# Optimization experiments

Measured on AMD Instinct MI355X. Metric: run time of the kernel, lower is better.

## Reference

```python
import jax, jax.numpy as jnp
import numpy as np


def setup_inputs() -> dict:
    key = jax.random.key(0)
    ks = jax.random.split(key, 9)
    B, S, D, E, I = 4, 2048, 1024, 8, 2048
    sd = 1.0 / np.sqrt(D)
    si = 1.0 / np.sqrt(I)
    return {
        "hidden_states": jax.random.normal(ks[0], (B, S, D), dtype=jnp.float32),
        "gate_w": jax.random.normal(ks[1], (D, E), dtype=jnp.float32) * sd,
        "expert_gate_w": jax.random.normal(ks[2], (E, D, I), dtype=jnp.float32) * sd,
        "expert_up_w": jax.random.normal(ks[3], (E, D, I), dtype=jnp.float32) * sd,
        "expert_down_w": jax.random.normal(ks[4], (E, I, D), dtype=jnp.float32) * si,
        "shared_gate_proj_w": jax.random.normal(ks[5], (D, I), dtype=jnp.float32) * sd,
        "shared_up_w": jax.random.normal(ks[6], (D, I), dtype=jnp.float32) * sd,
        "shared_down_w": jax.random.normal(ks[7], (I, D), dtype=jnp.float32) * si,
        "shared_expert_gate_w": jax.random.normal(ks[8], (D, 1), dtype=jnp.float32) * sd,
        "top_k": 2,
    }


def reference(hidden_states, gate_w, expert_gate_w, expert_up_w, expert_down_w,
              shared_gate_proj_w, shared_up_w, shared_down_w, shared_expert_gate_w,
              top_k):
    B, S, D = hidden_states.shape
    E = gate_w.shape[1]
    x = hidden_states.reshape(-1, D)            # [T, D]
    T = x.shape[0]

    # Router: softmax in fp32, top-k, dense per-token per-expert combine weights.
    gate_vals = x @ gate_w                      # [T, E]
    probs = jax.nn.softmax(gate_vals.astype(jnp.float32), axis=-1)
    top_w, top_i = jax.lax.top_k(probs, top_k)  # [T, K]
    dense_w = jnp.zeros((T, E), dtype=jnp.float32)
    dense_w = dense_w.at[jnp.arange(T)[:, None], top_i].set(top_w)
    dense_w = dense_w.astype(x.dtype)           # zero for unselected experts

    # All experts as batched SwiGLU GEMMs (tokens with zero weight contribute 0).
    g = jnp.einsum('td,edi->eti', x, expert_gate_w)
    u = jnp.einsum('td,edi->eti', x, expert_up_w)
    y = jnp.einsum('eti,eid->etd', jax.nn.silu(g) * u, expert_down_w)  # [E, T, D]
    moe_out = jnp.einsum('etd,te->td', y, dense_w)                      # [T, D]

    # Shared expert with sigmoid gate.
    shared = (jax.nn.silu(x @ shared_gate_proj_w) * (x @ shared_up_w)) @ shared_down_w
    shared = jax.nn.sigmoid(x @ shared_expert_gate_w) * shared

    final = (moe_out + shared).reshape(B, S, D)
    return final, gate_vals
```

## Files before the change

kernel.cpp:

```cpp
#include <hip/hip_runtime.h>

typedef __bf16 bf16x8 __attribute__((ext_vector_type(8)));
typedef float f32x4 __attribute__((ext_vector_type(4)));
typedef float f4 __attribute__((ext_vector_type(4)));
typedef unsigned short us8 __attribute__((ext_vector_type(8)));

#define T_TOK 8192
#define DDIM 1024
#define NEXP 8
#define IDIM 2048
#define NCH 1024
#define RROWS 17408
#define ROWS_TOT (T_TOK + RROWS)

__device__ __forceinline__ unsigned short f2bf(float f) {
    unsigned u = __float_as_uint(f);
    u += 0x7fffu + ((u >> 16) & 1u);
    return (unsigned short)(u >> 16);
}

#define GLDS(src, dst) __builtin_amdgcn_global_load_lds( \
    (const __attribute__((address_space(1))) void*)(src), \
    (__attribute__((address_space(3))) void*)(dst), 16, 0, 0)

__global__ __launch_bounds__(256) void router_kernel(
    const float* __restrict__ x, const float* __restrict__ gate_w,
    const float* __restrict__ sgw, float* __restrict__ gate_out,
    float* __restrict__ wdense, float* __restrict__ sgout)
{
    __shared__ float lgw[DDIM * NEXP];
    __shared__ float lsg[DDIM];
    int tid = threadIdx.x;
    for (int i = tid; i < (DDIM * NEXP) / 4; i += 256)
        ((f4*)lgw)[i] = ((const f4*)gate_w)[i];
    for (int i = tid; i < DDIM / 4; i += 256)
        ((f4*)lsg)[i] = ((const f4*)sgw)[i];
    __syncthreads();

    int wid = tid >> 6, l = tid & 63;
    int t = blockIdx.x * 4 + wid;

    float acc[NEXP];
#pragma unroll
    for (int e = 0; e < NEXP; e++) acc[e] = 0.f;
    float accs = 0.f;
    const float* xr = x + (size_t)t * DDIM;
#pragma unroll
    for (int j = 0; j < 4; j++) {
        int d0 = j * 256 + l * 4;
        f4 xv = *(const f4*)(xr + d0);
#pragma unroll
        for (int c = 0; c < 4; c++) {
            float xd = xv[c];
            int d = d0 + c;
#pragma unroll
            for (int e = 0; e < NEXP; e++) acc[e] += xd * lgw[d * NEXP + e];
            accs += xd * lsg[d];
        }
    }
#pragma unroll
    for (int off = 32; off > 0; off >>= 1) {
#pragma unroll
        for (int e = 0; e < NEXP; e++) acc[e] += __shfl_xor(acc[e], off);
        accs += __shfl_xor(accs, off);
    }
    if (l == 0) {
        float m = acc[0];
        for (int e = 1; e < NEXP; e++) m = fmaxf(m, acc[e]);
        float p[NEXP], s = 0.f;
        for (int e = 0; e < NEXP; e++) { p[e] = __expf(acc[e] - m); s += p[e]; }
        float inv = 1.f / s;
        int i1 = 0; float b1 = p[0];
        for (int e = 1; e < NEXP; e++) if (p[e] > b1) { b1 = p[e]; i1 = e; }
        int i2 = -1; float b2 = -1.f;
        for (int e = 0; e < NEXP; e++) if (e != i1 && p[e] > b2) { b2 = p[e]; i2 = e; }
        for (int e = 0; e < NEXP; e++) {
            gate_out[(size_t)t * NEXP + e] = acc[e];
            float w = (e == i1) ? b1 * inv : (e == i2) ? b2 * inv : 0.f;
            wdense[(size_t)t * NEXP + e] = w;
        }
        sgout[t] = 1.f / (1.f + __expf(-accs));
    }
}

__global__ __launch_bounds__(256) void bucket_kernel(
    const float* __restrict__ wdense, int* __restrict__ list,
    float* __restrict__ wl, int* __restrict__ cnt,
    int* __restrict__ te, int* __restrict__ tp)
{
    int e = blockIdx.x;
    int tid = threadIdx.x, wid = tid >> 6, l = tid & 63;
    __shared__ int wsum[4];
    int base = 0;
    int* le = list + (size_t)e * T_TOK;
    float* we = wl + (size_t)e * T_TOK;
    for (int t0 = 0; t0 < T_TOK; t0 += 256) {
        int tok = t0 + tid;
        float w = wdense[(size_t)tok * NEXP + e];
        bool f = w > 0.f;
        unsigned long long m = __ballot(f);
        int lp = __popcll(m & ((1ull << l) - 1ull));
        if (l == 0) wsum[wid] = __popcll(m);
        __syncthreads();
        int woff = 0;
#pragma unroll
        for (int i = 0; i < 4; i++) if (i < wid) woff += wsum[i];
        int btot = wsum[0] + wsum[1] + wsum[2] + wsum[3];
        if (f) {
            int pos = base + woff + lp;
            le[pos] = tok; we[pos] = w;
            int slot = 0;
            for (int e2 = 0; e2 < e; e2++)
                slot += (wdense[(size_t)tok * NEXP + e2] > 0.f) ? 1 : 0;
            te[tok * 2 + slot] = e;
            tp[tok * 2 + slot] = pos;
        }
        base += btot;
        __syncthreads();
    }
    if (tid == 0) cnt[e] = base;
    int align = (base + 255) & ~255;
    for (int i = base + tid; i < align; i += 256) { le[i] = 0; we[i] = 0.f; }
}

__global__ void scan_kernel(const int* __restrict__ cnt, int* __restrict__ offs)
{
    if (threadIdx.x == 0) {
        int o = 0;
        for (int e = 0; e < NEXP; e++) { offs[e] = o; o += (cnt[e] + 127) & ~127; }
    }
}

__global__ __launch_bounds__(256) void cvt_kernel(
    const float* __restrict__ in, unsigned short* __restrict__ out, int n8)
{
    int i = blockIdx.x * 256 + threadIdx.x;
    if (i >= n8) return;
    const f4* p = (const f4*)in + (size_t)i * 2;
    f4 a = p[0], b = p[1];
    us8 o;
#pragma unroll
    for (int k = 0; k < 4; k++) { o[k] = f2bf(a[k]); o[4 + k] = f2bf(b[k]); }
    *((us8*)out + i) = o;
}

__global__ __launch_bounds__(256) void wcvt_gu_kernel(
    const float* __restrict__ egw, const float* __restrict__ euw,
    const float* __restrict__ sgp, const float* __restrict__ sup,
    unsigned short* __restrict__ pool, int c0)
{
    int j = blockIdx.y;
    int e = j >> 1, s = j & 1;
    const float* src = (e < 8) ? ((s ? euw : egw) + (size_t)e * DDIM * IDIM)
                               : (s ? sup : sgp);
    unsigned short* dst = pool + (size_t)j * NCH * DDIM;
    int tpc = NCH / 64;
    int tci = blockIdx.x % tpc, tri = blockIdx.x / tpc;
    int r0 = tri * 64;
    int cl0 = tci * 64;
    int cg0 = c0 + cl0;

    __shared__ unsigned short lds[64][72];
    int t = threadIdx.x;
    int tr = t >> 4, tcc = (t & 15) * 4;
#pragma unroll
    for (int jj = 0; jj < 4; jj++) {
        int r = tr + jj * 16;
        f4 v = *(const f4*)(src + (size_t)(r0 + r) * IDIM + cg0 + tcc);
#pragma unroll
        for (int k = 0; k < 4; k++) lds[r][tcc + k] = f2bf(v[k]);
    }
    __syncthreads();
    int orow = t >> 2, ss = t & 3;
    us8 v0, v1;
#pragma unroll
    for (int i = 0; i < 8; i++) {
        v0[i] = lds[ss * 16 + i][orow];
        v1[i] = lds[ss * 16 + 8 + i][orow];
    }
    unsigned short* op = dst + (size_t)(cl0 + orow) * DDIM + r0 + ss * 16;
    *(us8*)op = v0; *(us8*)(op + 8) = v1;
}

__global__ __launch_bounds__(256) void wcvt_d_kernel(
    const float* __restrict__ edw, const float* __restrict__ sdw,
    unsigned short* __restrict__ pool)
{
    int j = blockIdx.y;
    const float* src = (j < 8) ? edw + (size_t)j * IDIM * DDIM : sdw;
    unsigned short* dst = pool + (size_t)j * DDIM * IDIM;
    int tpc = DDIM / 64;
    int tci = blockIdx.x % tpc, tri = blockIdx.x / tpc;
    int rg0 = tri * 64;
    int cg0 = tci * 64;

    __shared__ unsigned short lds[64][72];
    int t = threadIdx.x;
    int tr = t >> 4, tcc = (t & 15) * 4;
#pragma unroll
    for (int jj = 0; jj < 4; jj++) {
        int r = tr + jj * 16;
        f4 v = *(const f4*)(src + (size_t)(rg0 + r) * DDIM + cg0 + tcc);
#pragma unroll
        for (int k = 0; k < 4; k++) lds[r][tcc + k] = f2bf(v[k]);
    }
    __syncthreads();
    int orow = t >> 2, ss = t & 3;
    us8 v0, v1;
#pragma unroll
    for (int i = 0; i < 8; i++) {
        v0[i] = lds[ss * 16 + i][orow];
        v1[i] = lds[ss * 16 + 8 + i][orow];
    }
    unsigned short* op = dst + (size_t)(cg0 + orow) * IDIM + rg0 + ss * 16;
    *(us8*)op = v0; *(us8*)(op + 8) = v1;
}

__global__ __launch_bounds__(512, 2) void gemm_gateup8(
    const unsigned short* __restrict__ A, const unsigned short* __restrict__ pool,
    unsigned short* __restrict__ H, const int* __restrict__ listb,
    const int* __restrict__ cnt, const int* __restrict__ offs, int c0)
{
    int z = blockIdx.z;
    const unsigned short *Bg, *Bu; const int* lst; int count, rowb;
    if (z == 0) {
        Bg = pool + (size_t)16 * NCH * DDIM; Bu = pool + (size_t)17 * NCH * DDIM;
        lst = nullptr; count = T_TOK; rowb = 0;
    } else {
        int e = z - 1;
        Bg = pool + (size_t)(e * 2) * NCH * DDIM; Bu = pool + (size_t)(e * 2 + 1) * NCH * DDIM;
        lst = listb + (size_t)e * T_TOK; count = cnt[e]; rowb = T_TOK + offs[e];
    }
    int m0 = blockIdx.y * 256, n0 = blockIdx.x * 128;
    if (m0 >= count) return;
    int climit = (count + 127) & ~127;
    const int NT = DDIM / 64;

    __shared__ unsigned short lds[2][32768];

    int tid = threadIdx.x, wid = tid >> 6, l = tid & 63;
    int wm = wid >> 1, wn = wid & 1;
    int lr = l & 15, lkg = l >> 4;

    int sb = tid & 7, sr = tid >> 3;
    int sk = (sb ^ (sr & 7)) << 3;
    const unsigned short* pa[2][2];
#pragma unroll
    for (int h = 0; h < 2; h++)
#pragma unroll
        for (int j = 0; j < 2; j++) {
            int rr = m0 + h * 128 + j * 64 + sr;
            int ga = lst ? lst[rr] : rr;
            pa[h][j] = A + (size_t)ga * DDIM + sk;
        }
    const unsigned short* pbg = Bg + (size_t)(n0 + sr) * DDIM + sk;
    const unsigned short* pbu = Bu + (size_t)(n0 + sr) * DDIM + sk;

#define GU_ST_A(sbuf, h, t) { \
    GLDS(pa[h][0] + (t) * 64, (sbuf) + (h) * 8192 + tid * 8); \
    GLDS(pa[h][1] + (t) * 64, (sbuf) + (h) * 8192 + 4096 + tid * 8); }
#define GU_ST_BG(sbuf, t) { \
    GLDS(pbg + (t) * 64, (sbuf) + 16384 + tid * 8); \
    GLDS(pbg + (size_t)64 * DDIM + (t) * 64, (sbuf) + 16384 + 4096 + tid * 8); }
#define GU_ST_BU(sbuf, t) { \
    GLDS(pbu + (t) * 64, (sbuf) + 24576 + tid * 8); \
    GLDS(pbu + (size_t)64 * DDIM + (t) * 64, (sbuf) + 24576 + 4096 + tid * 8); }

    {
        unsigned short* s0 = &lds[0][0];
        GU_ST_A(s0, 0, 0); GU_ST_A(s0, 1, 0); GU_ST_BG(s0, 0); GU_ST_BU(s0, 0);
        unsigned short* s1 = &lds[1][0];
        GU_ST_A(s1, 0, 1); GU_ST_A(s1, 1, 1); GU_ST_BG(s1, 1); GU_ST_BU(s1, 1);
    }

    int xorc = (lr & 7) << 3;
    int kx0 = (lkg * 8) ^ xorc;
    int kx1 = (32 + lkg * 8) ^ xorc;
    int aoff[4], boff[4];
#pragma unroll
    for (int mf = 0; mf < 4; mf++) {
        int r = wm * 64 + mf * 16 + lr;
        aoff[mf] = (r >> 7) * 8192 + (r & 127) * 64;
    }
#pragma unroll
    for (int nf = 0; nf < 4; nf++)
        boff[nf] = 16384 + (wn * 64 + nf * 16 + lr) * 64;

    f32x4 zero = {0.f, 0.f, 0.f, 0.f};
    f32x4 accg[4][4], accu[4][4];
#pragma unroll
    for (int m = 0; m < 4; m++)
#pragma unroll
        for (int n = 0; n < 4; n++) { accg[m][n] = zero; accu[m][n] = zero; }

    bf16x8 a[2][2], bg[4][2], bu[4][2];

#pragma unroll 1
    for (int t = 0; t < NT; t++) {
        const unsigned short* cb = &lds[t & 1][0];
        unsigned short* sbuf = &lds[t & 1][0];
        bool stg = (t + 2 < NT);

        if (t == NT - 1) { asm volatile("s_waitcnt vmcnt(0)" ::: "memory"); }
        else             { asm volatile("s_waitcnt vmcnt(8)" ::: "memory"); }
        __builtin_amdgcn_s_barrier();
#pragma unroll
        for (int mf = 0; mf < 2; mf++) {
            a[mf][0] = *(const bf16x8*)(cb + aoff[mf] + kx0);
            a[mf][1] = *(const bf16x8*)(cb + aoff[mf] + kx1);
        }
#pragma unroll
        for (int nf = 0; nf < 2; nf++) {
            bg[nf][0] = *(const bf16x8*)(cb + boff[nf] + kx0);
            bg[nf][1] = *(const bf16x8*)(cb + boff[nf] + kx1);
            bu[nf][0] = *(const bf16x8*)(cb + boff[nf] + 8192 + kx0);
            bu[nf][1] = *(const bf16x8*)(cb + boff[nf] + 8192 + kx1);
        }
        __builtin_amdgcn_s_setprio(1);
#pragma unroll
        for (int kh = 0; kh < 2; kh++)
#pragma unroll
            for (int mf = 0; mf < 2; mf++)
#pragma unroll
                for (int nf = 0; nf < 2; nf++) {
                    accg[mf][nf] = __builtin_amdgcn_mfma_f32_16x16x32_bf16(a[mf][kh], bg[nf][kh], accg[mf][nf], 0, 0, 0);
                    accu[mf][nf] = __builtin_amdgcn_mfma_f32_16x16x32_bf16(a[mf][kh], bu[nf][kh], accu[mf][nf], 0, 0, 0);
                }
        __builtin_amdgcn_s_setprio(0);

        __builtin_amdgcn_s_barrier();
#pragma unroll
        for (int nf = 2; nf < 4; nf++) {
            bg[nf][0] = *(const bf16x8*)(cb + boff[nf] + kx0);
            bg[nf][1] = *(const bf16x8*)(cb + boff[nf] + kx1);
            bu[nf][0] = *(const bf16x8*)(cb + boff[nf] + 8192 + kx0);
            bu[nf][1] = *(const bf16x8*)(cb + boff[nf] + 8192 + kx1);
        }
        __builtin_amdgcn_s_setprio(1);
#pragma unroll
        for (int kh = 0; kh < 2; kh++)
#pragma unroll
            for (int mf = 0; mf < 2; mf++)
#pragma unroll
                for (int nf = 2; nf < 4; nf++) {
                    accg[mf][nf] = __builtin_amdgcn_mfma_f32_16x16x32_bf16(a[mf][kh], bg[nf][kh], accg[mf][nf], 0, 0, 0);
                    accu[mf][nf] = __builtin_amdgcn_mfma_f32_16x16x32_bf16(a[mf][kh], bu[nf][kh], accu[mf][nf], 0, 0, 0);
                }
        __builtin_amdgcn_s_setprio(0);

        __builtin_amdgcn_s_barrier();
#pragma unroll
        for (int mf = 0; mf < 2; mf++) {
            a[mf][0] = *(const bf16x8*)(cb + aoff[2 + mf] + kx0);
            a[mf][1] = *(const bf16x8*)(cb + aoff[2 + mf] + kx1);
        }
        if (stg) { GU_ST_BG(sbuf, t + 2); }
        __builtin_amdgcn_s_setprio(1);
#pragma unroll
        for (int kh = 0; kh < 2; kh++)
#pragma unroll
            for (int mf = 0; mf < 2; mf++)
#pragma unroll
                for (int nf = 0; nf < 2; nf++) {
                    accg[2 + mf][nf] = __builtin_amdgcn_mfma_f32_16x16x32_bf16(a[mf][kh], bg[nf][kh], accg[2 + mf][nf], 0, 0, 0);
                    accu[2 + mf][nf] = __builtin_amdgcn_mfma_f32_16x16x32_bf16(a[mf][kh], bu[nf][kh], accu[2 + mf][nf], 0, 0, 0);
                }
        __builtin_amdgcn_s_setprio(0);

        __builtin_amdgcn_s_barrier();
        if (stg) { GU_ST_BU(sbuf, t + 2); GU_ST_A(sbuf, 0, t + 2); GU_ST_A(sbuf, 1, t + 2); }
        __builtin_amdgcn_s_setprio(1);
#pragma unroll
        for (int kh = 0; kh < 2; kh++)
#pragma unroll
            for (int mf = 0; mf < 2; mf++)
#pragma unroll
                for (int nf = 2; nf < 4; nf++) {
                    accg[2 + mf][nf] = __builtin_amdgcn_mfma_f32_16x16x32_bf16(a[mf][kh], bg[nf][kh], accg[2 + mf][nf], 0, 0, 0);
                    accu[2 + mf][nf] = __builtin_amdgcn_mfma_f32_16x16x32_bf16(a[mf][kh], bu[nf][kh], accu[2 + mf][nf], 0, 0, 0);
                }
        __builtin_amdgcn_s_setprio(0);
    }

#pragma unroll
    for (int mf = 0; mf < 4; mf++) {
        int rbase = m0 + wm * 64 + mf * 16 + lkg * 4;
#pragma unroll
        for (int nf = 0; nf < 4; nf++) {
            int col = c0 + n0 + wn * 64 + nf * 16 + lr;
#pragma unroll
            for (int r = 0; r < 4; r++) {
                int rloc = rbase + r;
                if (rloc < climit) {
                    float g = accg[mf][nf][r], u = accu[mf][nf][r];
                    float hv = g * (1.f / (1.f + __expf(-g))) * u;
                    H[(size_t)(rowb + rloc) * IDIM + col] = f2bf(hv);
                }
            }
        }
    }
}

__global__ __launch_bounds__(512, 2) void gemm_down8(
    const unsigned short* __restrict__ H, const unsigned short* __restrict__ pool,
    unsigned short* __restrict__ Y,
    const float* __restrict__ wlb, const float* __restrict__ sgo,
    const int* __restrict__ cnt, const int* __restrict__ offs)
{
    int z = blockIdx.z;
    const unsigned short* B; const float* coef; int count, rowb;
    if (z == 0) {
        B = pool + (size_t)8 * DDIM * IDIM;
        coef = sgo; count = T_TOK; rowb = 0;
    } else {
        int e = z - 1;
        B = pool + (size_t)e * DDIM * IDIM;
        coef = wlb + (size_t)e * T_TOK;
        count = cnt[e]; rowb = T_TOK + offs[e];
    }
    int m0 = blockIdx.y * 256, n0 = blockIdx.x * 256;
    if (m0 >= count) return;
    int climit = (count + 127) & ~127;
    const int NT = IDIM / 64;

    __shared__ unsigned short lds[2][32768];

    int tid = threadIdx.x, wid = tid >> 6, l = tid & 63;
    int wm = wid >> 2, wn = wid & 3;
    int lr = l & 15, lkg = l >> 4;

    int sb = tid & 7, sr = tid >> 3;
    int sk = (sb ^ (sr & 7)) << 3;
    const unsigned short* pah = H + (size_t)(rowb + m0 + sr) * IDIM + sk;
    const unsigned short* pb  = B + (size_t)(n0 + sr) * IDIM + sk;

#define DN_ST_A(sbuf, h, t) { \
    GLDS(pah + (size_t)((h) * 128) * IDIM + (t) * 64, (sbuf) + (h) * 8192 + tid * 8); \
    GLDS(pah + (size_t)((h) * 128 + 64) * IDIM + (t) * 64, (sbuf) + (h) * 8192 + 4096 + tid * 8); }
#define DN_ST_B(sbuf, h, t) { \
    GLDS(pb + (size_t)((h) * 128) * IDIM + (t) * 64, (sbuf) + 16384 + (h) * 8192 + tid * 8); \
    GLDS(pb + (size_t)((h) * 128 + 64) * IDIM + (t) * 64, (sbuf) + 16384 + (h) * 8192 + 4096 + tid * 8); }

    {
        unsigned short* s0 = &lds[0][0];
        DN_ST_A(s0, 0, 0); DN_ST_A(s0, 1, 0); DN_ST_B(s0, 0, 0); DN_ST_B(s0, 1, 0);
        unsigned short* s1 = &lds[1][0];
        DN_ST_A(s1, 0, 1); DN_ST_A(s1, 1, 1); DN_ST_B(s1, 0, 1); DN_ST_B(s1, 1, 1);
    }

    int xorc = (lr & 7) << 3;
    int kx0 = (lkg * 8) ^ xorc;
    int kx1 = (32 + lkg * 8) ^ xorc;
    int aoff[8], boff[4];
#pragma unroll
    for (int mf = 0; mf < 8; mf++)
        aoff[mf] = wm * 8192 + (mf * 16 + lr) * 64;
#pragma unroll
    for (int nf = 0; nf < 4; nf++)
        boff[nf] = 16384 + (wn * 64 + nf * 16 + lr) * 64;

    f32x4 zero = {0.f, 0.f, 0.f, 0.f};
    f32x4 acc[8][4];
#pragma unroll
    for (int m = 0; m < 8; m++)
#pragma unroll
        for (int n = 0; n < 4; n++) acc[m][n] = zero;

    bf16x8 a[4][2], b[4][2];

#pragma unroll 1
    for (int t = 0; t < NT; t++) {
        const unsigned short* cb = &lds[t & 1][0];
        unsigned short* sbuf = &lds[t & 1][0];
        bool stg = (t + 2 < NT);

        if (t == NT - 1) { asm volatile("s_waitcnt vmcnt(0)" ::: "memory"); }
        else             { asm volatile("s_waitcnt vmcnt(8)" ::: "memory"); }
        __builtin_amdgcn_s_barrier();
#pragma unroll
        for (int mf = 0; mf < 4; mf++) {
            a[mf][0] = *(const bf16x8*)(cb + aoff[mf] + kx0);
            a[mf][1] = *(const bf16x8*)(cb + aoff[mf] + kx1);
        }
#pragma unroll
        for (int nf = 0; nf < 2; nf++) {
            b[nf][0] = *(const bf16x8*)(cb + boff[nf] + kx0);
            b[nf][1] = *(const bf16x8*)(cb + boff[nf] + kx1);
        }
        __builtin_amdgcn_s_setprio(1);
#pragma unroll
        for (int kh = 0; kh < 2; kh++)
#pragma unroll
            for (int mf = 0; mf < 4; mf++)
#pragma unroll
                for (int nf = 0; nf < 2; nf++)
                    acc[mf][nf] = __builtin_amdgcn_mfma_f32_16x16x32_bf16(a[mf][kh], b[nf][kh], acc[mf][nf], 0, 0, 0);
        __builtin_amdgcn_s_setprio(0);

        __builtin_amdgcn_s_barrier();
#pragma unroll
        for (int nf = 2; nf < 4; nf++) {
            b[nf][0] = *(const bf16x8*)(cb + boff[nf] + kx0);
            b[nf][1] = *(const bf16x8*)(cb + boff[nf] + kx1);
        }
        __builtin_amdgcn_s_setprio(1);
#pragma unroll
        for (int kh = 0; kh < 2; kh++)
#pragma unroll
            for (int mf = 0; mf < 4; mf++)
#pragma unroll
                for (int nf = 2; nf < 4; nf++)
                    acc[mf][nf] = __builtin_amdgcn_mfma_f32_16x16x32_bf16(a[mf][kh], b[nf][kh], acc[mf][nf], 0, 0, 0);
        __builtin_amdgcn_s_setprio(0);

        __builtin_amdgcn_s_barrier();
#pragma unroll
        for (int mf = 0; mf < 4; mf++) {
            a[mf][0] = *(const bf16x8*)(cb + aoff[4 + mf] + kx0);
            a[mf][1] = *(const bf16x8*)(cb + aoff[4 + mf] + kx1);
        }
        if (stg) { DN_ST_B(sbuf, 0, t + 2); }
        __builtin_amdgcn_s_setprio(1);
#pragma unroll
        for (int kh = 0; kh < 2; kh++)
#pragma unroll
            for (int mf = 0; mf < 4; mf++)
#pragma unroll
                for (int nf = 0; nf < 2; nf++)
                    acc[4 + mf][nf] = __builtin_amdgcn_mfma_f32_16x16x32_bf16(a[mf][kh], b[nf][kh], acc[4 + mf][nf], 0, 0, 0);
        __builtin_amdgcn_s_setprio(0);

        __builtin_amdgcn_s_barrier();
        if (stg) { DN_ST_B(sbuf, 1, t + 2); DN_ST_A(sbuf, 0, t + 2); DN_ST_A(sbuf, 1, t + 2); }
        __builtin_amdgcn_s_setprio(1);
#pragma unroll
        for (int kh = 0; kh < 2; kh++)
#pragma unroll
            for (int mf = 0; mf < 4; mf++)
#pragma unroll
                for (int nf = 2; nf < 4; nf++)
                    acc[4 + mf][nf] = __builtin_amdgcn_mfma_f32_16x16x32_bf16(a[mf][kh], b[nf][kh], acc[4 + mf][nf], 0, 0, 0);
        __builtin_amdgcn_s_setprio(0);
    }

#pragma unroll
    for (int mf = 0; mf < 8; mf++) {
        int rbase = m0 + wm * 128 + mf * 16 + lkg * 4;
        float cf[4];
#pragma unroll
        for (int r = 0; r < 4; r++) {
            int rloc = rbase + r;
            cf[r] = (rloc < climit) ? coef[rloc] : 0.f;
        }
#pragma unroll
        for (int nf = 0; nf < 4; nf++) {
            int col = n0 + wn * 64 + nf * 16 + lr;
#pragma unroll
            for (int r = 0; r < 4; r++) {
                int rloc = rbase + r;
                if (rloc < climit)
                    Y[(size_t)(rowb + rloc) * DDIM + col] = f2bf(cf[r] * acc[mf][nf][r]);
            }
        }
    }
}

__global__ __launch_bounds__(256) void combine_kernel(
    const unsigned short* __restrict__ Y, const int* __restrict__ te,
    const int* __restrict__ tp, const int* __restrict__ offs,
    float* __restrict__ out)
{
    int t = blockIdx.x * 2 + (threadIdx.x >> 7);
    int c = (threadIdx.x & 127) * 8;
    int e0 = te[2 * t], e1 = te[2 * t + 1];
    size_t r0 = (size_t)T_TOK + offs[e0] + tp[2 * t];
    size_t r1 = (size_t)T_TOK + offs[e1] + tp[2 * t + 1];

    us8 vs = *(const us8*)(Y + (size_t)t * DDIM + c);
    us8 v0 = *(const us8*)(Y + r0 * DDIM + c);
    us8 v1 = *(const us8*)(Y + r1 * DDIM + c);
    f4 o0, o1;
#pragma unroll
    for (int k = 0; k < 4; k++) {
        o0[k] = __uint_as_float((unsigned)vs[k] << 16)
              + __uint_as_float((unsigned)v0[k] << 16)
              + __uint_as_float((unsigned)v1[k] << 16);
        o1[k] = __uint_as_float((unsigned)vs[4 + k] << 16)
              + __uint_as_float((unsigned)v0[4 + k] << 16)
              + __uint_as_float((unsigned)v1[4 + k] << 16);
    }
    float* op = out + (size_t)t * DDIM + c;
    *(f4*)op = o0;
    *(f4*)(op + 4) = o1;
}

extern "C" void kernel_launch(void* const* d_in, const int* in_sizes, int n_in,
                              void* d_out, int out_size, void* d_ws, size_t ws_size,
                              hipStream_t stream)
{
    const float* x   = (const float*)d_in[0];
    const float* gw  = (const float*)d_in[1];
    const float* egw = (const float*)d_in[2];
    const float* euw = (const float*)d_in[3];
    const float* edw = (const float*)d_in[4];
    const float* sgp = (const float*)d_in[5];
    const float* sup = (const float*)d_in[6];
    const float* sdw = (const float*)d_in[7];
    const float* seg = (const float*)d_in[8];

    float* out0 = (float*)d_out;
    float* gate_out = out0 + (size_t)T_TOK * DDIM;

    char* ws = (char*)d_ws;
    auto take = [&](size_t bytes) { char* p = ws; ws += (bytes + 255) & ~(size_t)255; return p; };
    unsigned short* xb   = (unsigned short*)take((size_t)T_TOK * DDIM * 2);
    float* wdense = (float*)take((size_t)T_TOK * NEXP * 4);
    float* sgo    = (float*)take((size_t)T_TOK * 4);
    int*   list   = (int*)take((size_t)NEXP * T_TOK * 4);
    float* wl     = (float*)take((size_t)NEXP * T_TOK * 4);
    int*   cnt    = (int*)take(256);
    int*   offs   = (int*)take(256);
    int*   te     = (int*)take((size_t)T_TOK * 2 * 4);
    int*   tp     = (int*)take((size_t)T_TOK * 2 * 4);
    unsigned short* pool = (unsigned short*)take((size_t)18 * NCH * DDIM * 2);
    unsigned short* H    = (unsigned short*)take((size_t)ROWS_TOT * IDIM * 2);
    unsigned short* Y    = (unsigned short*)take((size_t)ROWS_TOT * DDIM * 2);

    router_kernel<<<T_TOK / 4, 256, 0, stream>>>(x, gw, seg, gate_out, wdense, sgo);
    bucket_kernel<<<NEXP, 256, 0, stream>>>(wdense, list, wl, cnt, te, tp);
    scan_kernel<<<1, 64, 0, stream>>>(cnt, offs);
    cvt_kernel<<<(T_TOK * DDIM / 8) / 256, 256, 0, stream>>>(x, xb, T_TOK * DDIM / 8);

    for (int c = 0; c < 2; c++) {
        int c0 = c * NCH;
        wcvt_gu_kernel<<<dim3((NCH / 64) * 16, 18), 256, 0, stream>>>(
            egw, euw, sgp, sup, pool, c0);
        gemm_gateup8<<<dim3(NCH / 128, T_TOK / 256, 9), 512, 0, stream>>>(
            xb, pool, H, list, cnt, offs, c0);
    }

    wcvt_d_kernel<<<dim3((IDIM / 64) * 16, 9), 256, 0, stream>>>(edw, sdw, pool);
    gemm_down8<<<dim3(DDIM / 256, T_TOK / 256, 9), 512, 0, stream>>>(
        H, pool, Y, wl, sgo, cnt, offs);

    combine_kernel<<<T_TOK / 2, 256, 0, stream>>>(Y, te, tp, offs, out0);
}
```

Baseline: 552.0 us.

## Shrink down-projection GEMM M-tile to 128 and relax launch bounds

Cuts the down-projection GEMM block tile from 256x256 to 128x256. That halves the accumulators and the A staging per block, simplifies the K-loop into two MFMA phases with a single staging point, and doubles the grid along M. Both GEMM kernels change launch_bounds min-blocks from 2 to 1, which lets the compiler use more registers. The aim is better load balance on the uneven per-expert token counts and less padding waste, at the cost of more B-tile reloads per output and possibly lower occupancy.

```diff
diff --git a/kernel.cpp b/kernel.cpp
--- a/kernel.cpp
+++ b/kernel.cpp
@@ -216,7 +216,7 @@
     *(us8*)op = v0; *(us8*)(op + 8) = v1;
 }
 
-__global__ __launch_bounds__(512, 2) void gemm_gateup8(
+__global__ __launch_bounds__(512, 1) void gemm_gateup8(
     const unsigned short* __restrict__ A, const unsigned short* __restrict__ pool,
     unsigned short* __restrict__ H, const int* __restrict__ listb,
     const int* __restrict__ cnt, const int* __restrict__ offs, int c0)
@@ -401,7 +401,7 @@
     }
 }
 
-__global__ __launch_bounds__(512, 2) void gemm_down8(
+__global__ __launch_bounds__(512, 1) void gemm_down8(
     const unsigned short* __restrict__ H, const unsigned short* __restrict__ pool,
     unsigned short* __restrict__ Y,
     const float* __restrict__ wlb, const float* __restrict__ sgo,
@@ -418,51 +418,52 @@
         coef = wlb + (size_t)e * T_TOK;
         count = cnt[e]; rowb = T_TOK + offs[e];
     }
-    int m0 = blockIdx.y * 256, n0 = blockIdx.x * 256;
+    int m0 = blockIdx.y * 128, n0 = blockIdx.x * 256;
     if (m0 >= count) return;
     int climit = (count + 127) & ~127;
     const int NT = IDIM / 64;
 
-    __shared__ unsigned short lds[2][32768];
+    __shared__ unsigned short lds[2][24576];
 
     int tid = threadIdx.x, wid = tid >> 6, l = tid & 63;
     int wm = wid >> 2, wn = wid & 3;
     int lr = l & 15, lkg = l >> 4;
 
-    int sb = tid & 7, sr = tid >> 3;
-    int sk = (sb ^ (sr & 7)) << 3;
+    int sr = tid >> 3;
+    int sk = ((tid & 7) ^ (sr & 7)) << 3;
     const unsigned short* pah = H + (size_t)(rowb + m0 + sr) * IDIM + sk;
     const unsigned short* pb  = B + (size_t)(n0 + sr) * IDIM + sk;
 
-#define DN_ST_A(sbuf, h, t) { \
-    GLDS(pah + (size_t)((h) * 128) * IDIM + (t) * 64, (sbuf) + (h) * 8192 + tid * 8); \
-    GLDS(pah + (size_t)((h) * 128 + 64) * IDIM + (t) * 64, (sbuf) + (h) * 8192 + 4096 + tid * 8); }
-#define DN_ST_B(sbuf, h, t) { \
-    GLDS(pb + (size_t)((h) * 128) * IDIM + (t) * 64, (sbuf) + 16384 + (h) * 8192 + tid * 8); \
-    GLDS(pb + (size_t)((h) * 128 + 64) * IDIM + (t) * 64, (sbuf) + 16384 + (h) * 8192 + 4096 + tid * 8); }
+#define DN_ST(sbuf, t) { \
+    GLDS(pah + (t) * 64, (sbuf) + tid * 8); \
+    GLDS(pah + (size_t)64 * IDIM + (t) * 64, (sbuf) + 4096 + tid * 8); \
+    GLDS(pb + (t) * 64, (sbuf) + 8192 + tid * 8); \
+    GLDS(pb + (size_t)64 * IDIM + (t) * 64, (sbuf) + 8192 + 4096 + tid * 8); \
+    GLDS(pb + (size_t)128 * IDIM + (t) * 64, (sbuf) + 16384 + tid * 8); \
+    GLDS(pb + (size_t)192 * IDIM + (t) * 64, (sbuf) + 16384 + 4096 + tid * 8); }
 
     {
         unsigned short* s0 = &lds[0][0];
-        DN_ST_A(s0, 0, 0); DN_ST_A(s0, 1, 0); DN_ST_B(s0, 0, 0); DN_ST_B(s0, 1, 0);
+        DN_ST(s0, 0);
         unsigned short* s1 = &lds[1][0];
-        DN_ST_A(s1, 0, 1); DN_ST_A(s1, 1, 1); DN_ST_B(s1, 0, 1); DN_ST_B(s1, 1, 1);
+        DN_ST(s1, 1);
     }
 
     int xorc = (lr & 7) << 3;
     int kx0 = (lkg * 8) ^ xorc;
     int kx1 = (32 + lkg * 8) ^ xorc;
-    int aoff[8], boff[4];
-#pragma unroll
-    for (int mf = 0; mf < 8; mf++)
-        aoff[mf] = wm * 8192 + (mf * 16 + lr) * 64;
+    int aoff[4], boff[4];
+#pragma unroll
+    for (int mf = 0; mf < 4; mf++)
+        aoff[mf] = (wm * 64 + mf * 16 + lr) * 64;
 #pragma unroll
     for (int nf = 0; nf < 4; nf++)
-        boff[nf] = 16384 + (wn * 64 + nf * 16 + lr) * 64;
+        boff[nf] = 8192 + (wn * 64 + nf * 16 + lr) * 64;
 
     f32x4 zero = {0.f, 0.f, 0.f, 0.f};
-    f32x4 acc[8][4];
-#pragma unroll
-    for (int m = 0; m < 8; m++)
+    f32x4 acc[4][4];
+#pragma unroll
+    for (int m = 0; m < 4; m++)
 #pragma unroll
         for (int n = 0; n < 4; n++) acc[m][n] = zero;
 
@@ -475,7 +476,7 @@
         bool stg = (t + 2 < NT);
 
         if (t == NT - 1) { asm volatile("s_waitcnt vmcnt(0)" ::: "memory"); }
-        else             { asm volatile("s_waitcnt vmcnt(8)" ::: "memory"); }
+        else             { asm volatile("s_waitcnt vmcnt(6)" ::: "memory"); }
         __builtin_amdgcn_s_barrier();
 #pragma unroll
         for (int mf = 0; mf < 4; mf++) {
@@ -483,7 +484,7 @@
             a[mf][1] = *(const bf16x8*)(cb + aoff[mf] + kx1);
         }
 #pragma unroll
-        for (int nf = 0; nf < 2; nf++) {
+        for (int nf = 0; nf < 4; nf++) {
             b[nf][0] = *(const bf16x8*)(cb + boff[nf] + kx0);
             b[nf][1] = *(const bf16x8*)(cb + boff[nf] + kx1);
         }
@@ -498,11 +499,7 @@
         __builtin_amdgcn_s_setprio(0);
 
         __builtin_amdgcn_s_barrier();
-#pragma unroll
-        for (int nf = 2; nf < 4; nf++) {
-            b[nf][0] = *(const bf16x8*)(cb + boff[nf] + kx0);
-            b[nf][1] = *(const bf16x8*)(cb + boff[nf] + kx1);
-        }
+        if (stg) { DN_ST(sbuf, t + 2); }
         __builtin_amdgcn_s_setprio(1);
 #pragma unroll
         for (int kh = 0; kh < 2; kh++)
@@ -512,40 +509,11 @@
                 for (int nf = 2; nf < 4; nf++)
                     acc[mf][nf] = __builtin_amdgcn_mfma_f32_16x16x32_bf16(a[mf][kh], b[nf][kh], acc[mf][nf], 0, 0, 0);
         __builtin_amdgcn_s_setprio(0);
-
-        __builtin_amdgcn_s_barrier();
-#pragma unroll
-        for (int mf = 0; mf < 4; mf++) {
-            a[mf][0] = *(const bf16x8*)(cb + aoff[4 + mf] + kx0);
-            a[mf][1] = *(const bf16x8*)(cb + aoff[4 + mf] + kx1);
-        }
-        if (stg) { DN_ST_B(sbuf, 0, t + 2); }
-        __builtin_amdgcn_s_setprio(1);
-#pragma unroll
-        for (int kh = 0; kh < 2; kh++)
-#pragma unroll
-            for (int mf = 0; mf < 4; mf++)
-#pragma unroll
-                for (int nf = 0; nf < 2; nf++)
-                    acc[4 + mf][nf] = __builtin_amdgcn_mfma_f32_16x16x32_bf16(a[mf][kh], b[nf][kh], acc[4 + mf][nf], 0, 0, 0);
-        __builtin_amdgcn_s_setprio(0);
-
-        __builtin_amdgcn_s_barrier();
-        if (stg) { DN_ST_B(sbuf, 1, t + 2); DN_ST_A(sbuf, 0, t + 2); DN_ST_A(sbuf, 1, t + 2); }
-        __builtin_amdgcn_s_setprio(1);
-#pragma unroll
-        for (int kh = 0; kh < 2; kh++)
-#pragma unroll
-            for (int mf = 0; mf < 4; mf++)
-#pragma unroll
-                for (int nf = 2; nf < 4; nf++)
-                    acc[4 + mf][nf] = __builtin_amdgcn_mfma_f32_16x16x32_bf16(a[mf][kh], b[nf][kh], acc[4 + mf][nf], 0, 0, 0);
-        __builtin_amdgcn_s_setprio(0);
-    }
-
-#pragma unroll
-    for (int mf = 0; mf < 8; mf++) {
-        int rbase = m0 + wm * 128 + mf * 16 + lkg * 4;
+    }
+
+#pragma unroll
+    for (int mf = 0; mf < 4; mf++) {
+        int rbase = m0 + wm * 64 + mf * 16 + lkg * 4;
         float cf[4];
 #pragma unroll
         for (int r = 0; r < 4; r++) {
@@ -640,7 +608,7 @@
     }
 
     wcvt_d_kernel<<<dim3((IDIM / 64) * 16, 9), 256, 0, stream>>>(edw, sdw, pool);
-    gemm_down8<<<dim3(DDIM / 256, T_TOK / 256, 9), 512, 0, stream>>>(
+    gemm_down8<<<dim3(DDIM / 256, T_TOK / 128, 9), 512, 0, stream>>>(
         H, pool, Y, wl, sgo, cnt, offs);
 
     combine_kernel<<<T_TOK / 2, 256, 0, stream>>>(Y, te, tp, offs, out0);
```

Result: slower. 574.8 us (+4.1%).

## Restructure GEMM main loops into barrier-gated phases with sched barriers and single occupancy

Applied to the files above, without the earlier changes.

Reorganises both the gate/up and down GEMM main loops into four phases. Each phase issues its LDS reads and then passes a barrier plus an lgkmcnt wait, with sched_barrier fences around it, before running MFMAs at raised priority. The vmcnt wait for the next stage moves to the end of each iteration, and global-to-LDS staging is regrouped so B loads come in one phase and A loads in another. Launch bounds drop from 2 to 1 blocks per CU, giving more registers per wave at the cost of occupancy. The aim is a deterministic ping-pong overlap between waves, but the stricter fences may serialise work.

```diff
diff --git a/kernel.cpp b/kernel.cpp
--- a/kernel.cpp
+++ b/kernel.cpp
@@ -22,6 +22,26 @@
 #define GLDS(src, dst) __builtin_amdgcn_global_load_lds( \
     (const __attribute__((address_space(1))) void*)(src), \
     (__attribute__((address_space(3))) void*)(dst), 16, 0, 0)
+
+#define PHASE_MID() do { \
+    __builtin_amdgcn_sched_barrier(0); \
+    __builtin_amdgcn_s_barrier(); \
+    asm volatile("s_waitcnt lgkmcnt(0)" ::: "memory"); \
+    __builtin_amdgcn_sched_barrier(0); \
+    __builtin_amdgcn_s_setprio(1); \
+} while (0)
+#define PHASE_END() do { \
+    __builtin_amdgcn_s_setprio(0); \
+    __builtin_amdgcn_sched_barrier(0); \
+    __builtin_amdgcn_s_barrier(); \
+} while (0)
+#define PHASE_END_GATE(stg) do { \
+    __builtin_amdgcn_s_setprio(0); \
+    __builtin_amdgcn_sched_barrier(0); \
+    if (stg) { asm volatile("s_waitcnt vmcnt(8)" ::: "memory"); } \
+    else     { asm volatile("s_waitcnt vmcnt(0)" ::: "memory"); } \
+    __builtin_amdgcn_s_barrier(); \
+} while (0)
 
 __global__ __launch_bounds__(256) void router_kernel(
     const float* __restrict__ x, const float* __restrict__ gate_w,
@@ -216,7 +236,7 @@
     *(us8*)op = v0; *(us8*)(op + 8) = v1;
 }
 
-__global__ __launch_bounds__(512, 2) void gemm_gateup8(
+__global__ __launch_bounds__(512, 1) void gemm_gateup8(
     const unsigned short* __restrict__ A, const unsigned short* __restrict__ pool,
     unsigned short* __restrict__ H, const int* __restrict__ listb,
     const int* __restrict__ cnt, const int* __restrict__ offs, int c0)
@@ -242,23 +262,23 @@
     int wm = wid >> 1, wn = wid & 1;
     int lr = l & 15, lkg = l >> 4;
 
-    int sb = tid & 7, sr = tid >> 3;
-    int sk = (sb ^ (sr & 7)) << 3;
-    const unsigned short* pa[2][2];
-#pragma unroll
-    for (int h = 0; h < 2; h++)
-#pragma unroll
-        for (int j = 0; j < 2; j++) {
-            int rr = m0 + h * 128 + j * 64 + sr;
-            int ga = lst ? lst[rr] : rr;
-            pa[h][j] = A + (size_t)ga * DDIM + sk;
-        }
+    int sr = tid >> 3;
+    int sk = ((tid & 7) ^ (sr & 7)) << 3;
+    const unsigned short* pa[4];
+#pragma unroll
+    for (int h = 0; h < 4; h++) {
+        int rr = m0 + h * 64 + sr;
+        int ga = lst ? lst[rr] : rr;
+        pa[h] = A + (size_t)ga * DDIM + sk;
+    }
     const unsigned short* pbg = Bg + (size_t)(n0 + sr) * DDIM + sk;
     const unsigned short* pbu = Bu + (size_t)(n0 + sr) * DDIM + sk;
 
-#define GU_ST_A(sbuf, h, t) { \
-    GLDS(pa[h][0] + (t) * 64, (sbuf) + (h) * 8192 + tid * 8); \
-    GLDS(pa[h][1] + (t) * 64, (sbuf) + (h) * 8192 + 4096 + tid * 8); }
+#define GU_ST_A(sbuf, t) { \
+    GLDS(pa[0] + (t) * 64, (sbuf) + tid * 8); \
+    GLDS(pa[1] + (t) * 64, (sbuf) + 4096 + tid * 8); \
+    GLDS(pa[2] + (t) * 64, (sbuf) + 8192 + tid * 8); \
+    GLDS(pa[3] + (t) * 64, (sbuf) + 12288 + tid * 8); }
 #define GU_ST_BG(sbuf, t) { \
     GLDS(pbg + (t) * 64, (sbuf) + 16384 + tid * 8); \
     GLDS(pbg + (size_t)64 * DDIM + (t) * 64, (sbuf) + 16384 + 4096 + tid * 8); }
@@ -268,20 +288,20 @@
 
     {
         unsigned short* s0 = &lds[0][0];
-        GU_ST_A(s0, 0, 0); GU_ST_A(s0, 1, 0); GU_ST_BG(s0, 0); GU_ST_BU(s0, 0);
+        GU_ST_A(s0, 0); GU_ST_BG(s0, 0); GU_ST_BU(s0, 0);
         unsigned short* s1 = &lds[1][0];
-        GU_ST_A(s1, 0, 1); GU_ST_A(s1, 1, 1); GU_ST_BG(s1, 1); GU_ST_BU(s1, 1);
-    }
+        GU_ST_A(s1, 1); GU_ST_BG(s1, 1); GU_ST_BU(s1, 1);
+    }
+    asm volatile("s_waitcnt vmcnt(8)" ::: "memory");
+    __builtin_amdgcn_s_barrier();
 
     int xorc = (lr & 7) << 3;
     int kx0 = (lkg * 8) ^ xorc;
     int kx1 = (32 + lkg * 8) ^ xorc;
     int aoff[4], boff[4];
 #pragma unroll
-    for (int mf = 0; mf < 4; mf++) {
-        int r = wm * 64 + mf * 16 + lr;
-        aoff[mf] = (r >> 7) * 8192 + (r & 127) * 64;
-    }
+    for (int mf = 0; mf < 4; mf++)
+        aoff[mf] = (wm * 64 + mf * 16 + lr) * 64;
 #pragma unroll
     for (int nf = 0; nf < 4; nf++)
         boff[nf] = 16384 + (wn * 64 + nf * 16 + lr) * 64;
@@ -301,85 +321,67 @@
         unsigned short* sbuf = &lds[t & 1][0];
         bool stg = (t + 2 < NT);
 
-        if (t == NT - 1) { asm volatile("s_waitcnt vmcnt(0)" ::: "memory"); }
-        else             { asm volatile("s_waitcnt vmcnt(8)" ::: "memory"); }
-        __builtin_amdgcn_s_barrier();
 #pragma unroll
         for (int mf = 0; mf < 2; mf++) {
             a[mf][0] = *(const bf16x8*)(cb + aoff[mf] + kx0);
             a[mf][1] = *(const bf16x8*)(cb + aoff[mf] + kx1);
         }
 #pragma unroll
-        for (int nf = 0; nf < 2; nf++) {
+        for (int nf = 0; nf < 4; nf++) {
             bg[nf][0] = *(const bf16x8*)(cb + boff[nf] + kx0);
             bg[nf][1] = *(const bf16x8*)(cb + boff[nf] + kx1);
+        }
+        PHASE_MID();
+#pragma unroll
+        for (int kh = 0; kh < 2; kh++)
+#pragma unroll
+            for (int mf = 0; mf < 2; mf++)
+#pragma unroll
+                for (int nf = 0; nf < 4; nf++)
+                    accg[mf][nf] = __builtin_amdgcn_mfma_f32_16x16x32_bf16(a[mf][kh], bg[nf][kh], accg[mf][nf], 0, 0, 0);
+        PHASE_END();
+
+#pragma unroll
+        for (int nf = 0; nf < 4; nf++) {
             bu[nf][0] = *(const bf16x8*)(cb + boff[nf] + 8192 + kx0);
             bu[nf][1] = *(const bf16x8*)(cb + boff[nf] + 8192 + kx1);
         }
-        __builtin_amdgcn_s_setprio(1);
+        PHASE_MID();
 #pragma unroll
         for (int kh = 0; kh < 2; kh++)
 #pragma unroll
             for (int mf = 0; mf < 2; mf++)
 #pragma unroll
-                for (int nf = 0; nf < 2; nf++) {
-                    accg[mf][nf] = __builtin_amdgcn_mfma_f32_16x16x32_bf16(a[mf][kh], bg[nf][kh], accg[mf][nf], 0, 0, 0);
+                for (int nf = 0; nf < 4; nf++)
                     accu[mf][nf] = __builtin_amdgcn_mfma_f32_16x16x32_bf16(a[mf][kh], bu[nf][kh], accu[mf][nf], 0, 0, 0);
-                }
-        __builtin_amdgcn_s_setprio(0);
-
-        __builtin_amdgcn_s_barrier();
-#pragma unroll
-        for (int nf = 2; nf < 4; nf++) {
-            bg[nf][0] = *(const bf16x8*)(cb + boff[nf] + kx0);
-            bg[nf][1] = *(const bf16x8*)(cb + boff[nf] + kx1);
-            bu[nf][0] = *(const bf16x8*)(cb + boff[nf] + 8192 + kx0);
-            bu[nf][1] = *(const bf16x8*)(cb + boff[nf] + 8192 + kx1);
-        }
-        __builtin_amdgcn_s_setprio(1);
-#pragma unroll
-        for (int kh = 0; kh < 2; kh++)
-#pragma unroll
-            for (int mf = 0; mf < 2; mf++)
-#pragma unroll
-                for (int nf = 2; nf < 4; nf++) {
-                    accg[mf][nf] = __builtin_amdgcn_mfma_f32_16x16x32_bf16(a[mf][kh], bg[nf][kh], accg[mf][nf], 0, 0, 0);
-                    accu[mf][nf] = __builtin_amdgcn_mfma_f32_16x16x32_bf16(a[mf][kh], bu[nf][kh], accu[mf][nf], 0, 0, 0);
-                }
-        __builtin_amdgcn_s_setprio(0);
-
-        __builtin_amdgcn_s_barrier();
+        PHASE_END();
+
 #pragma unroll
         for (int mf = 0; mf < 2; mf++) {
             a[mf][0] = *(const bf16x8*)(cb + aoff[2 + mf] + kx0);
             a[mf][1] = *(const bf16x8*)(cb + aoff[2 + mf] + kx1);
         }
-        if (stg) { GU_ST_BG(sbuf, t + 2); }
-        __builtin_amdgcn_s_setprio(1);
+        if (stg) { GU_ST_BG(sbuf, t + 2); GU_ST_BU(sbuf, t + 2); }
+        PHASE_MID();
 #pragma unroll
         for (int kh = 0; kh < 2; kh++)
 #pragma unroll
             for (int mf = 0; mf < 2; mf++)
 #pragma unroll
-                for (int nf = 0; nf < 2; nf++) {
+                for (int nf = 0; nf < 4; nf++)
                     accg[2 + mf][nf] = __builtin_amdgcn_mfma_f32_16x16x32_bf16(a[mf][kh], bg[nf][kh], accg[2 + mf][nf], 0, 0, 0);
+        PHASE_END();
+
+        if (stg) { GU_ST_A(sbuf, t + 2); }
+        PHASE_MID();
+#pragma unroll
+        for (int kh = 0; kh < 2; kh++)
+#pragma unroll
+            for (int mf = 0; mf < 2; mf++)
+#pragma unroll
+                for (int nf = 0; nf < 4; nf++)
                     accu[2 + mf][nf] = __builtin_amdgcn_mfma_f32_16x16x32_bf16(a[mf][kh], bu[nf][kh], accu[2 + mf][nf], 0, 0, 0);
-                }
-        __builtin_amdgcn_s_setprio(0);
-
-        __builtin_amdgcn_s_barrier();
-        if (stg) { GU_ST_BU(sbuf, t + 2); GU_ST_A(sbuf, 0, t + 2); GU_ST_A(sbuf, 1, t + 2); }
-        __builtin_amdgcn_s_setprio(1);
-#pragma unroll
-        for (int kh = 0; kh < 2; kh++)
-#pragma unroll
-            for (int mf = 0; mf < 2; mf++)
-#pragma unroll
-                for (int nf = 2; nf < 4; nf++) {
-                    accg[2 + mf][nf] = __builtin_amdgcn_mfma_f32_16x16x32_bf16(a[mf][kh], bg[nf][kh], accg[2 + mf][nf], 0, 0, 0);
-                    accu[2 + mf][nf] = __builtin_amdgcn_mfma_f32_16x16x32_bf16(a[mf][kh], bu[nf][kh], accu[2 + mf][nf], 0, 0, 0);
-                }
-        __builtin_amdgcn_s_setprio(0);
+        PHASE_END_GATE(stg);
     }
 
 #pragma unroll
@@ -401,7 +403,7 @@
     }
 }
 
-__global__ __launch_bounds__(512, 2) void gemm_down8(
+__global__ __launch_bounds__(512, 1) void gemm_down8(
     const unsigned short* __restrict__ H, const unsigned short* __restrict__ pool,
     unsigned short* __restrict__ Y,
     const float* __restrict__ wlb, const float* __restrict__ sgo,
@@ -429,24 +431,30 @@
     int wm = wid >> 2, wn = wid & 3;
     int lr = l & 15, lkg = l >> 4;
 
-    int sb = tid & 7, sr = tid >> 3;
-    int sk = (sb ^ (sr & 7)) << 3;
+    int sr = tid >> 3;
+    int sk = ((tid & 7) ^ (sr & 7)) << 3;
     const unsigned short* pah = H + (size_t)(rowb + m0 + sr) * IDIM + sk;
     const unsigned short* pb  = B + (size_t)(n0 + sr) * IDIM + sk;
 
-#define DN_ST_A(sbuf, h, t) { \
-    GLDS(pah + (size_t)((h) * 128) * IDIM + (t) * 64, (sbuf) + (h) * 8192 + tid * 8); \
-    GLDS(pah + (size_t)((h) * 128 + 64) * IDIM + (t) * 64, (sbuf) + (h) * 8192 + 4096 + tid * 8); }
-#define DN_ST_B(sbuf, h, t) { \
-    GLDS(pb + (size_t)((h) * 128) * IDIM + (t) * 64, (sbuf) + 16384 + (h) * 8192 + tid * 8); \
-    GLDS(pb + (size_t)((h) * 128 + 64) * IDIM + (t) * 64, (sbuf) + 16384 + (h) * 8192 + 4096 + tid * 8); }
+#define DN_ST_A(sbuf, t) { \
+    GLDS(pah + (t) * 64, (sbuf) + tid * 8); \
+    GLDS(pah + (size_t)64 * IDIM + (t) * 64, (sbuf) + 4096 + tid * 8); \
+    GLDS(pah + (size_t)128 * IDIM + (t) * 64, (sbuf) + 8192 + tid * 8); \
+    GLDS(pah + (size_t)192 * IDIM + (t) * 64, (sbuf) + 12288 + tid * 8); }
+#define DN_ST_B(sbuf, t) { \
+    GLDS(pb + (t) * 64, (sbuf) + 16384 + tid * 8); \
+    GLDS(pb + (size_t)64 * IDIM + (t) * 64, (sbuf) + 16384 + 4096 + tid * 8); \
+    GLDS(pb + (size_t)128 * IDIM + (t) * 64, (sbuf) + 16384 + 8192 + tid * 8); \
+    GLDS(pb + (size_t)192 * IDIM + (t) * 64, (sbuf) + 16384 + 12288 + tid * 8); }
 
     {
         unsigned short* s0 = &lds[0][0];
-        DN_ST_A(s0, 0, 0); DN_ST_A(s0, 1, 0); DN_ST_B(s0, 0, 0); DN_ST_B(s0, 1, 0);
+        DN_ST_A(s0, 0); DN_ST_B(s0, 0);
         unsigned short* s1 = &lds[1][0];
-        DN_ST_A(s1, 0, 1); DN_ST_A(s1, 1, 1); DN_ST_B(s1, 0, 1); DN_ST_B(s1, 1, 1);
-    }
+        DN_ST_A(s1, 1); DN_ST_B(s1, 1);
+    }
+    asm volatile("s_waitcnt vmcnt(8)" ::: "memory");
+    __builtin_amdgcn_s_barrier();
 
     int xorc = (lr & 7) << 3;
     int kx0 = (lkg * 8) ^ xorc;
@@ -454,7 +462,7 @@
     int aoff[8], boff[4];
 #pragma unroll
     for (int mf = 0; mf < 8; mf++)
-        aoff[mf] = wm * 8192 + (mf * 16 + lr) * 64;
+        aoff[mf] = (wm * 128 + mf * 16 + lr) * 64;
 #pragma unroll
     for (int nf = 0; nf < 4; nf++)
         boff[nf] = 16384 + (wn * 64 + nf * 16 + lr) * 64;
@@ -474,9 +482,6 @@
         unsigned short* sbuf = &lds[t & 1][0];
         bool stg = (t + 2 < NT);
 
-        if (t == NT - 1) { asm volatile("s_waitcnt vmcnt(0)" ::: "memory"); }
-        else             { asm volatile("s_waitcnt vmcnt(8)" ::: "memory"); }
-        __builtin_amdgcn_s_barrier();
 #pragma unroll
         for (int mf = 0; mf < 4; mf++) {
             a[mf][0] = *(const bf16x8*)(cb + aoff[mf] + kx0);
@@ -487,7 +492,7 @@
             b[nf][0] = *(const bf16x8*)(cb + boff[nf] + kx0);
             b[nf][1] = *(const bf16x8*)(cb + boff[nf] + kx1);
         }
-        __builtin_amdgcn_s_setprio(1);
+        PHASE_MID();
 #pragma unroll
         for (int kh = 0; kh < 2; kh++)
 #pragma unroll
@@ -495,15 +500,14 @@
 #pragma unroll
                 for (int nf = 0; nf < 2; nf++)
                     acc[mf][nf] = __builtin_amdgcn_mfma_f32_16x16x32_bf16(a[mf][kh], b[nf][kh], acc[mf][nf], 0, 0, 0);
-        __builtin_amdgcn_s_setprio(0);
-
-        __builtin_amdgcn_s_barrier();
+        PHASE_END();
+
 #pragma unroll
         for (int nf = 2; nf < 4; nf++) {
             b[nf][0] = *(const bf16x8*)(cb + boff[nf] + kx0);
             b[nf][1] = *(const bf16x8*)(cb + boff[nf] + kx1);
         }
-        __builtin_amdgcn_s_setprio(1);
+        PHASE_MID();
 #pragma unroll
         for (int kh = 0; kh < 2; kh++)
 #pragma unroll
@@ -511,16 +515,15 @@
 #pragma unroll
                 for (int nf = 2; nf < 4; nf++)
                     acc[mf][nf] = __builtin_amdgcn_mfma_f32_16x16x32_bf16(a[mf][kh], b[nf][kh], acc[mf][nf], 0, 0, 0);
-        __builtin_amdgcn_s_setprio(0);
-
-        __builtin_amdgcn_s_barrier();
+        PHASE_END();
+
 #pragma unroll
         for (int mf = 0; mf < 4; mf++) {
             a[mf][0] = *(const bf16x8*)(cb + aoff[4 + mf] + kx0);
             a[mf][1] = *(const bf16x8*)(cb + aoff[4 + mf] + kx1);
         }
-        if (stg) { DN_ST_B(sbuf, 0, t + 2); }
-        __builtin_amdgcn_s_setprio(1);
+        if (stg) { DN_ST_B(sbuf, t + 2); }
+        PHASE_MID();
 #pragma unroll
         for (int kh = 0; kh < 2; kh++)
 #pragma unroll
@@ -528,11 +531,10 @@
 #pragma unroll
                 for (int nf = 0; nf < 2; nf++)
                     acc[4 + mf][nf] = __builtin_amdgcn_mfma_f32_16x16x32_bf16(a[mf][kh], b[nf][kh], acc[4 + mf][nf], 0, 0, 0);
-        __builtin_amdgcn_s_setprio(0);
-
-        __builtin_amdgcn_s_barrier();
-        if (stg) { DN_ST_B(sbuf, 1, t + 2); DN_ST_A(sbuf, 0, t + 2); DN_ST_A(sbuf, 1, t + 2); }
-        __builtin_amdgcn_s_setprio(1);
+        PHASE_END();
+
+        if (stg) { DN_ST_A(sbuf, t + 2); }
+        PHASE_MID();
 #pragma unroll
         for (int kh = 0; kh < 2; kh++)
 #pragma unroll
@@ -540,7 +542,7 @@
 #pragma unroll
                 for (int nf = 2; nf < 4; nf++)
                     acc[4 + mf][nf] = __builtin_amdgcn_mfma_f32_16x16x32_bf16(a[mf][kh], b[nf][kh], acc[4 + mf][nf], 0, 0, 0);
-        __builtin_amdgcn_s_setprio(0);
+        PHASE_END_GATE(stg);
     }
 
 #pragma unroll
```

Measured after the change: 574.2 us. +4.0%, slower.
